# Optimization experiments

Measured on AMD Instinct MI355X. Metric: run time of the kernel, lower is better.

## Reference

```python
import jax, jax.numpy as jnp
import numpy as np

B, NE, E, MULT = 16384, 32, 128, 2
H = MULT * E  # hidden dim per expert


def setup_inputs() -> dict:
    key = jax.random.key(0)
    ks = jax.random.split(key, 6)
    features = jax.random.normal(ks[0], (B, NE, E), dtype=jnp.float32)
    target_features = jax.random.normal(ks[1], (B, NE, E), dtype=jnp.float32)
    # Stacked per-expert params (PyTorch Linear default init scale ~ 1/sqrt(fan_in))
    W1 = jax.random.normal(ks[2], (NE, E, H), dtype=jnp.float32) / np.sqrt(E)
    b1 = jax.random.normal(ks[3], (NE, H), dtype=jnp.float32) * 0.01
    W2 = jax.random.normal(ks[4], (NE, H, E), dtype=jnp.float32) / np.sqrt(H)
    b2 = jax.random.normal(ks[5], (NE, E), dtype=jnp.float32) * 0.01
    return {"features": features, "target_features": target_features,
            "W1": W1, "b1": b1, "W2": W2, "b2": b2}


def reference(features, target_features, W1, b1, W2, b2):
    # Batched grouped MLP over experts: [B, NE, E] x [NE, E, H] -> [B, NE, H]
    h = jnp.einsum('bne,neh->bnh', features, W1) + b1
    h = jax.nn.gelu(h, approximate=False)  # torch nn.GELU default = exact erf
    pred = jnp.einsum('bnh,nhe->bne', h, W2) + b2
    # sum_e mse_loss(pred[:,e], target[:,e]) / NE == mean over all elements
    return jnp.mean((pred - target_features) ** 2)
```

## Files before the change

### kernel.cpp

```cpp
#include <hip/hip_runtime.h>

constexpr int kB  = 16384;
constexpr int kNE = 32;
constexpr int kE  = 128;
constexpr int kH  = 256;
constexpr int MT  = 64;

typedef __attribute__((ext_vector_type(8))) short short8;
typedef __attribute__((ext_vector_type(4))) float float4v;

__device__ __forceinline__ unsigned short f2bf(float x) {
  unsigned int u = __float_as_uint(x);
  u += 0x7FFFu + ((u >> 16) & 1u);
  return (unsigned short)(u >> 16);
}

__device__ __forceinline__ unsigned int cvt_pk_bf16(float lo, float hi) {
  unsigned int r;
  asm("v_cvt_pk_bf16_f32 %0, %1, %2" : "=v"(r) : "v"(lo), "v"(hi));
  return r;
}

__device__ __forceinline__ float gelu_f(float x) {
  float x2 = x * x;
  float w = x * fmaf(x2, -0.10294428f, -2.30220795f);
  float z = __builtin_amdgcn_exp2f(w);
  return x * __builtin_amdgcn_rcpf(1.0f + z);
}

__device__ __forceinline__ void load_lds16(const unsigned short* g, unsigned short* l) {
  __builtin_amdgcn_global_load_lds(
      (const __attribute__((address_space(1))) unsigned int*)g,
      (__attribute__((address_space(3))) unsigned int*)l, 16, 0, 0);
}

__global__ __launch_bounds__(256)
void prep_weights(const float* __restrict__ W1, const float* __restrict__ W2,
                  unsigned short* __restrict__ W1F, unsigned short* __restrict__ W2F)
{
  const int n    = blockIdx.x;
  const int lane = threadIdx.x & 63;
  const int wv   = threadIdx.x >> 6;
  const int q = lane >> 4, col = lane & 15;
  const int fb = blockIdx.z * 4 + wv;
  const int c  = fb >> 4;
  if (blockIdx.y == 0) {
    const int kt = (fb >> 2) & 3, t = fb & 3;
    const float* src = W1 + (size_t)n * kE * kH
                          + (size_t)(kt * 32 + q * 8) * kH + (c * 64 + t * 16 + col);
    unsigned short* dst = W1F + (size_t)n * (kH * kE) + ((size_t)fb * 64 + lane) * 8;
    short8 v;
#pragma unroll
    for (int j = 0; j < 8; ++j) v[j] = (short)f2bf(src[(size_t)j * kH]);
    *(short8*)dst = v;
  } else {
    const int kt = (fb >> 3) & 1, je = fb & 7;
    const float* src = W2 + (size_t)n * kH * kE
                          + (size_t)(c * 64 + kt * 32 + q * 8) * kE + (je * 16 + col);
    unsigned short* dst = W2F + (size_t)n * (kE * kH) + ((size_t)fb * 64 + lane) * 8;
    short8 v;
#pragma unroll
    for (int j = 0; j < 8; ++j) v[j] = (short)f2bf(src[(size_t)j * kE]);
    *(short8*)dst = v;
  }
}

__global__ __launch_bounds__(256, 4)
void distill_moe_mse(const float* __restrict__ features,
                     const float* __restrict__ target,
                     const unsigned short* __restrict__ W1F,
                     const float* __restrict__ b1,
                     const unsigned short* __restrict__ W2F,
                     const float* __restrict__ b2,
                     float* __restrict__ out)
{
  __shared__ __align__(16) unsigned short sW1[8192];
  __shared__ __align__(16) unsigned short sW2[8192];

  const int tid  = threadIdx.x;
  const int lane = tid & 63;
  const int w    = tid >> 6;
  const int q    = lane >> 4;
  const int col  = lane & 15;
  const int n    = blockIdx.y;
  const int m    = blockIdx.x * MT + 16 * w + col;

  const float* arow = features + ((size_t)m * kNE + n) * kE;
  short8 areg[4];
#pragma unroll
  for (int kt = 0; kt < 4; ++kt) {
    float4v f0 = *(const float4v*)(arow + kt * 32 + q * 8);
    float4v f1 = *(const float4v*)(arow + kt * 32 + q * 8 + 4);
    union { unsigned int u[4]; short8 s; } pk;
    pk.u[0] = cvt_pk_bf16(f0.x, f0.y);
    pk.u[1] = cvt_pk_bf16(f0.z, f0.w);
    pk.u[2] = cvt_pk_bf16(f1.x, f1.y);
    pk.u[3] = cvt_pk_bf16(f1.z, f1.w);
    areg[kt] = pk.s;
  }

  float4v acc2[8];
#pragma unroll
  for (int je = 0; je < 8; ++je) acc2[je] = (float4v){0.f, 0.f, 0.f, 0.f};

  const unsigned short* W1n = W1F + (size_t)n * (kH * kE);
  const unsigned short* W2n = W2F + (size_t)n * (kE * kH);
  const float* b1n = b1 + n * kH;

  for (int c = 0; c < 4; ++c) {
    if (c) __syncthreads();
    {
      const unsigned short* g1 = W1n + c * 8192;
      const unsigned short* g2 = W2n + c * 8192;
#pragma unroll
      for (int i = 0; i < 4; ++i) {
        int seg = i * 4 + w;
        load_lds16(g1 + seg * 512 + lane * 8, &sW1[seg * 512]);
        load_lds16(g2 + seg * 512 + lane * 8, &sW2[seg * 512]);
      }
    }
    __syncthreads();

    float4v acc1[4];
#pragma unroll
    for (int t = 0; t < 4; ++t) acc1[t] = (float4v){0.f, 0.f, 0.f, 0.f};
#pragma unroll
    for (int kt = 0; kt < 4; ++kt) {
#pragma unroll
      for (int t = 0; t < 4; ++t) {
        short8 wf = *(const short8*)&sW1[(kt * 4 + t) * 512 + lane * 8];
        acc1[t] = __builtin_amdgcn_mfma_f32_16x16x32_bf16(wf, areg[kt], acc1[t], 0, 0, 0);
      }
    }

    unsigned int p[4][2];
    const float* bc = b1n + c * 64;
#pragma unroll
    for (int t = 0; t < 4; ++t) {
      float4v bias = *(const float4v*)(bc + t * 16 + q * 4);
      float g0 = gelu_f(acc1[t][0] + bias.x);
      float g1 = gelu_f(acc1[t][1] + bias.y);
      float g2 = gelu_f(acc1[t][2] + bias.z);
      float g3 = gelu_f(acc1[t][3] + bias.w);
      p[t][0] = cvt_pk_bf16(g0, g1);
      p[t][1] = cvt_pk_bf16(g2, g3);
    }

    short8 bfrag[2];
#pragma unroll
    for (int k2 = 0; k2 < 2; ++k2) {
      union { unsigned int u[4]; short8 s; } bf;
#pragma unroll
      for (int s = 0; s < 2; ++s) {
        auto uv = __builtin_amdgcn_permlane32_swap(p[2 * k2][s], p[2 * k2 + 1][s], false, false);
        auto mm = __builtin_amdgcn_permlane16_swap((unsigned int)uv[0], (unsigned int)uv[1], false, false);
        bf.u[s]     = (unsigned int)mm[0];
        bf.u[2 + s] = (unsigned int)mm[1];
      }
      bfrag[k2] = bf.s;
    }

#pragma unroll
    for (int k2 = 0; k2 < 2; ++k2) {
#pragma unroll
      for (int je = 0; je < 8; ++je) {
        short8 wf = *(const short8*)&sW2[(k2 * 8 + je) * 512 + lane * 8];
        acc2[je] = __builtin_amdgcn_mfma_f32_16x16x32_bf16(wf, bfrag[k2], acc2[je], 0, 0, 0);
      }
    }
  }

  const float* trow = target + ((size_t)m * kNE + n) * kE;
  const float* b2n  = b2 + n * kE;
  float local = 0.f;
#pragma unroll
  for (int je = 0; je < 8; ++je) {
    float4v tg = *(const float4v*)(trow + je * 16 + q * 4);
    float4v bb = *(const float4v*)(b2n + je * 16 + q * 4);
#pragma unroll
    for (int r = 0; r < 4; ++r) {
      float d = acc2[je][r] + bb[r] - tg[r];
      local += d * d;
    }
  }
#pragma unroll
  for (int off = 32; off > 0; off >>= 1)
    local += __shfl_down(local, off, 64);

  __syncthreads();
  float* sRedF = (float*)sW1;
  if (lane == 0) sRedF[w] = local;
  __syncthreads();
  if (tid == 0)
    atomicAdd(out, (sRedF[0] + sRedF[1] + sRedF[2] + sRedF[3]) *
                       (1.0f / ((float)kB * (float)kNE * (float)kE)));
}

extern "C" void kernel_launch(void* const* d_in, const int* in_sizes, int n_in,
                              void* d_out, int out_size, void* d_ws, size_t ws_size,
                              hipStream_t stream) {
  const float* features = (const float*)d_in[0];
  const float* target   = (const float*)d_in[1];
  const float* W1       = (const float*)d_in[2];
  const float* b1       = (const float*)d_in[3];
  const float* W2       = (const float*)d_in[4];
  const float* b2       = (const float*)d_in[5];
  float* out = (float*)d_out;

  unsigned short* W1F = (unsigned short*)d_ws;
  unsigned short* W2F = W1F + (size_t)kNE * kH * kE;

  hipMemsetAsync(out, 0, sizeof(float), stream);

  {
    dim3 grid(kNE, 2, 16);
    prep_weights<<<grid, dim3(256), 0, stream>>>(W1, W2, W1F, W2F);
  }
  {
    dim3 grid(kB / MT, kNE);
    distill_moe_mse<<<grid, dim3(256), 0, stream>>>(features, target, W1F, b1, W2F, b2, out);
  }
}
```

Before: 574.0 us.

## Double-buffer weight chunks and double rows per block with grid swizzle

Each block now handles 128 rows as two 64-row subtiles, so every weight fragment read from LDS feeds two MFMAs. The hidden dimension is split into eight 32-wide chunks, held in a double-buffered LDS ring and prefetched two chunks ahead with explicit vmcnt waits, so global-to-LDS loads overlap compute. b1 is cached in LDS, the grid order is swizzled, and MFMA sections raise wave priority. The goal is to cut weight reload traffic and barrier stalls. The cost is more registers (launch bounds drop from 4 to 3 blocks) and half as many blocks.

```diff
diff --git a/kernel.cpp b/kernel.cpp
--- a/kernel.cpp
+++ b/kernel.cpp
@@ -4,7 +4,8 @@
 constexpr int kNE = 32;
 constexpr int kE  = 128;
 constexpr int kH  = 256;
-constexpr int MT  = 64;
+constexpr int MT  = 128;
+constexpr int NCH = 8;
 
 typedef __attribute__((ext_vector_type(8))) short short8;
 typedef __attribute__((ext_vector_type(4))) float float4v;
@@ -42,22 +43,22 @@
   const int lane = threadIdx.x & 63;
   const int wv   = threadIdx.x >> 6;
   const int q = lane >> 4, col = lane & 15;
-  const int fb = blockIdx.z * 4 + wv;
-  const int c  = fb >> 4;
+  const int g = blockIdx.z * 4 + wv;
+  const int c = g >> 3;
   if (blockIdx.y == 0) {
-    const int kt = (fb >> 2) & 3, t = fb & 3;
+    const int kt = (g >> 1) & 3, t = g & 1;
     const float* src = W1 + (size_t)n * kE * kH
-                          + (size_t)(kt * 32 + q * 8) * kH + (c * 64 + t * 16 + col);
-    unsigned short* dst = W1F + (size_t)n * (kH * kE) + ((size_t)fb * 64 + lane) * 8;
+                          + (size_t)(kt * 32 + q * 8) * kH + (c * 32 + t * 16 + col);
+    unsigned short* dst = W1F + (size_t)n * (kH * kE) + ((size_t)g * 64 + lane) * 8;
     short8 v;
 #pragma unroll
     for (int j = 0; j < 8; ++j) v[j] = (short)f2bf(src[(size_t)j * kH]);
     *(short8*)dst = v;
   } else {
-    const int kt = (fb >> 3) & 1, je = fb & 7;
+    const int je = g & 7;
     const float* src = W2 + (size_t)n * kH * kE
-                          + (size_t)(c * 64 + kt * 32 + q * 8) * kE + (je * 16 + col);
-    unsigned short* dst = W2F + (size_t)n * (kE * kH) + ((size_t)fb * 64 + lane) * 8;
+                          + (size_t)(c * 32 + q * 8) * kE + (je * 16 + col);
+    unsigned short* dst = W2F + (size_t)n * (kE * kH) + ((size_t)g * 64 + lane) * 8;
     short8 v;
 #pragma unroll
     for (int j = 0; j < 8; ++j) v[j] = (short)f2bf(src[(size_t)j * kE]);
@@ -65,7 +66,7 @@
   }
 }
 
-__global__ __launch_bounds__(256, 4)
+__global__ __launch_bounds__(256, 3)
 void distill_moe_mse(const float* __restrict__ features,
                      const float* __restrict__ target,
                      const unsigned short* __restrict__ W1F,
@@ -74,125 +75,166 @@
                      const float* __restrict__ b2,
                      float* __restrict__ out)
 {
-  __shared__ __align__(16) unsigned short sW1[8192];
-  __shared__ __align__(16) unsigned short sW2[8192];
+  __shared__ __align__(16) unsigned short sW[2][8192];
+  __shared__ __align__(16) float sB1[kH];
+  __shared__ float sRed[4];
 
   const int tid  = threadIdx.x;
   const int lane = tid & 63;
   const int w    = tid >> 6;
   const int q    = lane >> 4;
   const int col  = lane & 15;
-  const int n    = blockIdx.y;
-  const int m    = blockIdx.x * MT + 16 * w + col;
-
-  const float* arow = features + ((size_t)m * kNE + n) * kE;
-  short8 areg[4];
-#pragma unroll
-  for (int kt = 0; kt < 4; ++kt) {
-    float4v f0 = *(const float4v*)(arow + kt * 32 + q * 8);
-    float4v f1 = *(const float4v*)(arow + kt * 32 + q * 8 + 4);
-    union { unsigned int u[4]; short8 s; } pk;
-    pk.u[0] = cvt_pk_bf16(f0.x, f0.y);
-    pk.u[1] = cvt_pk_bf16(f0.z, f0.w);
-    pk.u[2] = cvt_pk_bf16(f1.x, f1.y);
-    pk.u[3] = cvt_pk_bf16(f1.z, f1.w);
-    areg[kt] = pk.s;
-  }
-
-  float4v acc2[8];
-#pragma unroll
-  for (int je = 0; je < 8; ++je) acc2[je] = (float4v){0.f, 0.f, 0.f, 0.f};
+
+  const int bid = blockIdx.y * gridDim.x + blockIdx.x;
+  const int swz = (bid & 7) * (kNE * (kB / MT) / 8) + (bid >> 3);
+  const int n   = swz >> 7;
+  const int b0  = (swz & 127) * MT;
+  const int m0  = b0 + 16 * w + col;
 
   const unsigned short* W1n = W1F + (size_t)n * (kH * kE);
   const unsigned short* W2n = W2F + (size_t)n * (kE * kH);
   const float* b1n = b1 + n * kH;
-
-  for (int c = 0; c < 4; ++c) {
-    if (c) __syncthreads();
-    {
-      const unsigned short* g1 = W1n + c * 8192;
-      const unsigned short* g2 = W2n + c * 8192;
-#pragma unroll
-      for (int i = 0; i < 4; ++i) {
-        int seg = i * 4 + w;
-        load_lds16(g1 + seg * 512 + lane * 8, &sW1[seg * 512]);
-        load_lds16(g2 + seg * 512 + lane * 8, &sW2[seg * 512]);
-      }
-    }
-    __syncthreads();
-
-    float4v acc1[4];
-#pragma unroll
-    for (int t = 0; t < 4; ++t) acc1[t] = (float4v){0.f, 0.f, 0.f, 0.f};
+  const float* b2n = b2 + n * kE;
+
+  short8 areg[2][4];
+#pragma unroll
+  for (int mt = 0; mt < 2; ++mt) {
+    const float* arow = features + ((size_t)(m0 + mt * 64) * kNE + n) * kE;
 #pragma unroll
     for (int kt = 0; kt < 4; ++kt) {
-#pragma unroll
-      for (int t = 0; t < 4; ++t) {
-        short8 wf = *(const short8*)&sW1[(kt * 4 + t) * 512 + lane * 8];
-        acc1[t] = __builtin_amdgcn_mfma_f32_16x16x32_bf16(wf, areg[kt], acc1[t], 0, 0, 0);
-      }
-    }
-
-    unsigned int p[4][2];
-    const float* bc = b1n + c * 64;
-#pragma unroll
-    for (int t = 0; t < 4; ++t) {
-      float4v bias = *(const float4v*)(bc + t * 16 + q * 4);
-      float g0 = gelu_f(acc1[t][0] + bias.x);
-      float g1 = gelu_f(acc1[t][1] + bias.y);
-      float g2 = gelu_f(acc1[t][2] + bias.z);
-      float g3 = gelu_f(acc1[t][3] + bias.w);
-      p[t][0] = cvt_pk_bf16(g0, g1);
-      p[t][1] = cvt_pk_bf16(g2, g3);
-    }
+      float4v f0 = *(const float4v*)(arow + kt * 32 + q * 8);
+      float4v f1 = *(const float4v*)(arow + kt * 32 + q * 8 + 4);
+      union { unsigned int u[4]; short8 s; } pk;
+      pk.u[0] = cvt_pk_bf16(f0.x, f0.y);
+      pk.u[1] = cvt_pk_bf16(f0.z, f0.w);
+      pk.u[2] = cvt_pk_bf16(f1.x, f1.y);
+      pk.u[3] = cvt_pk_bf16(f1.z, f1.w);
+      areg[mt][kt] = pk.s;
+    }
+  }
+
+  if (tid < 64) {
+    float4v bv = *(const float4v*)(b1n + tid * 4);
+    *(float4v*)&sB1[tid * 4] = bv;
+  }
+
+  float4v acc2[2][8];
+#pragma unroll
+  for (int mt = 0; mt < 2; ++mt)
+#pragma unroll
+    for (int je = 0; je < 8; ++je) acc2[mt][je] = (float4v){0.f, 0.f, 0.f, 0.f};
+
+  __syncthreads();
+
+  auto stage = [&](int buf, int c) {
+    const unsigned short* g1 = W1n + c * 4096;
+    const unsigned short* g2 = W2n + c * 4096;
+#pragma unroll
+    for (int i = 0; i < 2; ++i) {
+      int s = i * 4 + w;
+      load_lds16(g1 + s * 512 + lane * 8, &sW[buf][s * 512]);
+      load_lds16(g2 + s * 512 + lane * 8, &sW[buf][4096 + s * 512]);
+    }
+  };
+
+  stage(0, 0);
+  stage(1, 1);
+
+#pragma unroll
+  for (int c = 0; c < NCH; ++c) {
+    if (c < NCH - 1) asm volatile("s_waitcnt vmcnt(4)" ::: "memory");
+    else             asm volatile("s_waitcnt vmcnt(0)" ::: "memory");
+    __builtin_amdgcn_sched_barrier(0);
+    __builtin_amdgcn_s_barrier();
+    __builtin_amdgcn_sched_barrier(0);
+
+    const unsigned short* w1c = &sW[c & 1][0];
+    const unsigned short* w2c = &sW[c & 1][4096];
+
+    float4v acc1[2][2];
+#pragma unroll
+    for (int mt = 0; mt < 2; ++mt)
+#pragma unroll
+      for (int t = 0; t < 2; ++t) acc1[mt][t] = (float4v){0.f, 0.f, 0.f, 0.f};
+
+    __builtin_amdgcn_s_setprio(1);
+#pragma unroll
+    for (int kt = 0; kt < 4; ++kt) {
+#pragma unroll
+      for (int t = 0; t < 2; ++t) {
+        short8 wf = *(const short8*)&w1c[(kt * 2 + t) * 512 + lane * 8];
+#pragma unroll
+        for (int mt = 0; mt < 2; ++mt)
+          acc1[mt][t] = __builtin_amdgcn_mfma_f32_16x16x32_bf16(wf, areg[mt][kt], acc1[mt][t], 0, 0, 0);
+      }
+    }
+    __builtin_amdgcn_s_setprio(0);
 
     short8 bfrag[2];
 #pragma unroll
-    for (int k2 = 0; k2 < 2; ++k2) {
+    for (int mt = 0; mt < 2; ++mt) {
+      unsigned int p[2][2];
+#pragma unroll
+      for (int t = 0; t < 2; ++t) {
+        float4v bias = *(const float4v*)&sB1[c * 32 + t * 16 + q * 4];
+        float g0 = gelu_f(acc1[mt][t][0] + bias.x);
+        float g1 = gelu_f(acc1[mt][t][1] + bias.y);
+        float g2 = gelu_f(acc1[mt][t][2] + bias.z);
+        float g3 = gelu_f(acc1[mt][t][3] + bias.w);
+        p[t][0] = cvt_pk_bf16(g0, g1);
+        p[t][1] = cvt_pk_bf16(g2, g3);
+      }
       union { unsigned int u[4]; short8 s; } bf;
 #pragma unroll
-      for (int s = 0; s < 2; ++s) {
-        auto uv = __builtin_amdgcn_permlane32_swap(p[2 * k2][s], p[2 * k2 + 1][s], false, false);
+      for (int s2 = 0; s2 < 2; ++s2) {
+        auto uv = __builtin_amdgcn_permlane32_swap(p[0][s2], p[1][s2], false, false);
         auto mm = __builtin_amdgcn_permlane16_swap((unsigned int)uv[0], (unsigned int)uv[1], false, false);
-        bf.u[s]     = (unsigned int)mm[0];
-        bf.u[2 + s] = (unsigned int)mm[1];
-      }
-      bfrag[k2] = bf.s;
-    }
-
-#pragma unroll
-    for (int k2 = 0; k2 < 2; ++k2) {
-#pragma unroll
-      for (int je = 0; je < 8; ++je) {
-        short8 wf = *(const short8*)&sW2[(k2 * 8 + je) * 512 + lane * 8];
-        acc2[je] = __builtin_amdgcn_mfma_f32_16x16x32_bf16(wf, bfrag[k2], acc2[je], 0, 0, 0);
-      }
-    }
-  }
-
-  const float* trow = target + ((size_t)m * kNE + n) * kE;
-  const float* b2n  = b2 + n * kE;
+        bf.u[s2]     = (unsigned int)mm[0];
+        bf.u[2 + s2] = (unsigned int)mm[1];
+      }
+      bfrag[mt] = bf.s;
+    }
+
+    __builtin_amdgcn_s_setprio(1);
+#pragma unroll
+    for (int je = 0; je < 8; ++je) {
+      short8 wf = *(const short8*)&w2c[je * 512 + lane * 8];
+#pragma unroll
+      for (int mt = 0; mt < 2; ++mt)
+        acc2[mt][je] = __builtin_amdgcn_mfma_f32_16x16x32_bf16(wf, bfrag[mt], acc2[mt][je], 0, 0, 0);
+    }
+    __builtin_amdgcn_s_setprio(0);
+
+    asm volatile("s_waitcnt lgkmcnt(0)" ::: "memory");
+    __builtin_amdgcn_sched_barrier(0);
+    __builtin_amdgcn_s_barrier();
+    __builtin_amdgcn_sched_barrier(0);
+    if (c + 2 < NCH) stage(c & 1, c + 2);
+  }
+
   float local = 0.f;
 #pragma unroll
   for (int je = 0; je < 8; ++je) {
-    float4v tg = *(const float4v*)(trow + je * 16 + q * 4);
     float4v bb = *(const float4v*)(b2n + je * 16 + q * 4);
 #pragma unroll
-    for (int r = 0; r < 4; ++r) {
-      float d = acc2[je][r] + bb[r] - tg[r];
-      local += d * d;
+    for (int mt = 0; mt < 2; ++mt) {
+      const float* trow = target + ((size_t)(m0 + mt * 64) * kNE + n) * kE;
+      float4v tg = *(const float4v*)(trow + je * 16 + q * 4);
+#pragma unroll
+      for (int r = 0; r < 4; ++r) {
+        float d = acc2[mt][je][r] + bb[r] - tg[r];
+        local += d * d;
+      }
     }
   }
 #pragma unroll
   for (int off = 32; off > 0; off >>= 1)
     local += __shfl_down(local, off, 64);
 
-  __syncthreads();
-  float* sRedF = (float*)sW1;
-  if (lane == 0) sRedF[w] = local;
+  if (lane == 0) sRed[w] = local;
   __syncthreads();
   if (tid == 0)
-    atomicAdd(out, (sRedF[0] + sRedF[1] + sRedF[2] + sRedF[3]) *
+    atomicAdd(out, (sRed[0] + sRed[1] + sRed[2] + sRed[3]) *
                        (1.0f / ((float)kB * (float)kNE * (float)kE)));
 }
 
```

Measured after the change: 540.8 us. -5.8%, faster.
